# Optimization experiments

Hardware: AMD Instinct MI355X
Metric: run time of the kernel (lower is better)

## Reference

```python
import jax, jax.numpy as jnp
import numpy as np

HIDDEN = 1024
NUM_HEAD = 16
HEAD_DIM = HIDDEN // NUM_HEAD


def setup_inputs() -> dict:
    key = jax.random.key(0)
    ks = jax.random.split(key, 12)
    bs, seq = 4, 2048
    inp = {
        'srcQ': jax.random.normal(ks[0], (bs, seq, HIDDEN), jnp.float32),
        'srcK': jax.random.normal(ks[1], (bs, seq, HIDDEN), jnp.float32),
        'srcV': jax.random.normal(ks[2], (bs, seq, HIDDEN), jnp.float32),
        'mask': jnp.ones((bs, 1, 1, seq), jnp.int32),
        'Wq': jax.random.normal(ks[3], (HIDDEN, HIDDEN), jnp.float32) * 0.02,
        'bq': jnp.zeros((HIDDEN,), jnp.float32),
        'Wk': jax.random.normal(ks[4], (HIDDEN, HIDDEN), jnp.float32) * 0.02,
        'bk': jnp.zeros((HIDDEN,), jnp.float32),
        'Wv': jax.random.normal(ks[5], (HIDDEN, HIDDEN), jnp.float32) * 0.02,
        'bv': jnp.zeros((HIDDEN,), jnp.float32),
        'Wo': jax.random.normal(ks[6], (HIDDEN, HIDDEN), jnp.float32) * 0.02,
        'bo': jnp.zeros((HIDDEN,), jnp.float32),
    }
    return inp


def _split_heads(x):
    # [bs, seq, hidden] -> [bs, num_head, seq, head_dim]
    bs, seq, _ = x.shape
    return x.reshape(bs, seq, NUM_HEAD, HEAD_DIM).transpose(0, 2, 1, 3)


def reference(srcQ, srcK, srcV, mask, Wq, bq, Wk, bk, Wv, bv, Wo, bo):
    Q = _split_heads(srcQ @ Wq + bq)
    K = _split_heads(srcK @ Wk + bk)
    V = _split_heads(srcV @ Wv + bv)
    # NOTE: original module applies NO 1/sqrt(d) scaling (scale tensor unused)
    scores = jnp.einsum('bhqd,bhkd->bhqk', Q, K)
    scores = jnp.where(mask == 0, jnp.float32(-10000.0), scores)
    attn = jax.nn.softmax(scores, axis=-1)  # dropout is identity in eval
    out = jnp.einsum('bhqk,bhkd->bhqd', attn, V)
    bs, _, seq, _ = out.shape
    out = out.transpose(0, 2, 1, 3).reshape(bs, seq, HIDDEN)
    return out @ Wo + bo
```

## Files before the change

kernel.cpp:

```cpp
#include <hip/hip_runtime.h>

typedef short bf16x8 __attribute__((ext_vector_type(8)));
typedef short bf16x4 __attribute__((ext_vector_type(4)));
typedef float f32x4 __attribute__((ext_vector_type(4)));
typedef unsigned short ushort8 __attribute__((ext_vector_type(8)));
typedef unsigned short ushort4v __attribute__((ext_vector_type(4)));
typedef unsigned int uint4v __attribute__((ext_vector_type(4)));
typedef float float4v __attribute__((ext_vector_type(4)));

#define LOG2E 1.4426950408889634f
#define MASKED_VAL -14426.950408889634f

__device__ __forceinline__ unsigned short f2bf(float f) {
  unsigned u = __builtin_bit_cast(unsigned, f);
  u = u + 0x7fffu + ((u >> 16) & 1u);
  return (unsigned short)(u >> 16);
}

__device__ __forceinline__ unsigned pk2(float a, float b) {
  unsigned r;
  asm("v_cvt_pk_bf16_f32 %0, %1, %2" : "=v"(r) : "v"(a), "v"(b));
  return r;
}

__device__ __forceinline__ float exp2a(float x) {
  float r;
  asm("v_exp_f32 %0, %1" : "=v"(r) : "v"(x));
  return r;
}

__device__ __forceinline__ void gload16(const void* g, void* l) {
  __builtin_amdgcn_global_load_lds(
      (const __attribute__((address_space(1))) unsigned int*)g,
      (__attribute__((address_space(3))) unsigned int*)l, 16, 0, 0);
}

__global__ __launch_bounds__(256) void transpose_w4(const float* __restrict__ W0,
                                                    const float* __restrict__ W1,
                                                    const float* __restrict__ W2,
                                                    const float* __restrict__ W3,
                                                    unsigned short* __restrict__ Wt) {
  __shared__ float tile[32][33];
  const int z = blockIdx.z;
  const float* W = (z == 0) ? W0 : (z == 1) ? W1 : (z == 2) ? W2 : W3;
  unsigned short* o = Wt + (size_t)z * (1 << 20);
  int bx = blockIdx.x * 32;
  int by = blockIdx.y * 32;
  int tx = threadIdx.x & 31;
  int ty = threadIdx.x >> 5;
#pragma unroll
  for (int j = 0; j < 32; j += 8)
    tile[ty + j][tx] = W[(size_t)(by + ty + j) * 1024 + bx + tx];
  __syncthreads();
#pragma unroll
  for (int j = 0; j < 32; j += 8)
    o[(size_t)(bx + ty + j) * 1024 + by + tx] = f2bf(tile[tx][ty + j]);
}

__global__ __launch_bounds__(256, 3) void gemm_qkv(
    const float* __restrict__ srcQ, const float* __restrict__ srcK,
    const float* __restrict__ srcV, const unsigned short* __restrict__ Wt,
    const float* __restrict__ bq, const float* __restrict__ bk,
    const float* __restrict__ bv, unsigned short* __restrict__ Qb,
    unsigned short* __restrict__ Kb, unsigned short* __restrict__ Vt) {
  __shared__ __align__(16) unsigned short As[3][128 * 32];
  __shared__ __align__(16) unsigned short Bs[3][128 * 32];
  const int K = 1024, N = 1024;
  const int chunk = blockIdx.x >> 9;
  const int inner = blockIdx.x & 511;
  const int x = inner & 7, i = inner >> 3;
  const int bm = (x << 3) + (i >> 3);
  const int bn = i & 7;
  const float* Af = (chunk == 0) ? srcQ : (chunk == 1) ? srcK : srcV;
  const unsigned short* Bt = Wt + (size_t)chunk * (1 << 20);
  const float* bias = (chunk == 0) ? bq : (chunk == 1) ? bk : bv;
  const float scale = (chunk == 0) ? LOG2E : 1.0f;
  const int t = threadIdx.x;
  const int lane = t & 63, wid = t >> 6;
  const int wr = wid >> 1, wc = wid & 1;
  const int lr = lane & 15, lg = lane >> 4;
  f32x4 acc[4][4] = {};
  const size_t baseA = (size_t)(bm * 128) * K;
  const size_t baseB = (size_t)(bn * 128) * K;
  const int c0 = t, c1 = t + 256;
  const size_t a0off = baseA + (size_t)(c0 >> 2) * K + (c0 & 3) * 8;
  const size_t a1off = baseA + (size_t)(c1 >> 2) * K + (c1 & 3) * 8;
  const size_t b0off = baseB + (size_t)(c0 >> 2) * K + (c0 & 3) * 8;
  const size_t b1off = baseB + (size_t)(c1 >> 2) * K + (c1 & 3) * 8;

  unsigned short* pA0 = &As[0][0];
  unsigned short* pA1 = &As[1][0];
  unsigned short* pA2 = &As[2][0];
  unsigned short* pB0 = &Bs[0][0];
  unsigned short* pB1 = &Bs[1][0];
  unsigned short* pB2 = &Bs[2][0];
  float4v fE[4], fO[4];

  auto loadA = [&](float4v* f, int ks) {
    f[0] = *(const float4v*)&Af[a0off + ks];
    f[1] = *(const float4v*)&Af[a0off + ks + 4];
    f[2] = *(const float4v*)&Af[a1off + ks];
    f[3] = *(const float4v*)&Af[a1off + ks + 4];
  };
  auto writeA = [&](const float4v* f, unsigned short* dst) {
    uint4v w0, w1;
    w0[0] = pk2(f[0][0], f[0][1]); w0[1] = pk2(f[0][2], f[0][3]);
    w0[2] = pk2(f[1][0], f[1][1]); w0[3] = pk2(f[1][2], f[1][3]);
    w1[0] = pk2(f[2][0], f[2][1]); w1[1] = pk2(f[2][2], f[2][3]);
    w1[2] = pk2(f[3][0], f[3][1]); w1[3] = pk2(f[3][2], f[3][3]);
    *(uint4v*)&dst[c0 * 8] = w0;
    *(uint4v*)&dst[c1 * 8] = w1;
  };
  auto compute = [&]() {
    bf16x8 a[4], b[4];
#pragma unroll
    for (int m = 0; m < 4; ++m)
      a[m] = *(const bf16x8*)&pA0[(wr * 64 + 16 * m + lr) * 32 + lg * 8];
#pragma unroll
    for (int n = 0; n < 4; ++n)
      b[n] = *(const bf16x8*)&pB0[(wc * 64 + 16 * n + lr) * 32 + lg * 8];
    __builtin_amdgcn_s_setprio(1);
#pragma unroll
    for (int m = 0; m < 4; ++m)
#pragma unroll
      for (int n = 0; n < 4; ++n)
        acc[m][n] = __builtin_amdgcn_mfma_f32_16x16x32_bf16(a[m], b[n], acc[m][n], 0, 0, 0);
    __builtin_amdgcn_s_setprio(0);
  };
  auto rotate = [&]() {
    unsigned short* ta = pA0; pA0 = pA1; pA1 = pA2; pA2 = ta;
    unsigned short* tb = pB0; pB0 = pB1; pB1 = pB2; pB2 = tb;
  };

  gload16(&Bt[b0off], &pB0[c0 * 8]);
  gload16(&Bt[b1off], &pB0[c1 * 8]);
  loadA(fE, 0);
  gload16(&Bt[b0off + 32], &pB1[c0 * 8]);
  gload16(&Bt[b1off + 32], &pB1[c1 * 8]);
  loadA(fO, 32);
  writeA(fE, pA0);
  asm volatile("s_waitcnt lgkmcnt(0)" ::: "memory");
  __builtin_amdgcn_s_barrier();

  for (int it = 0; it < 16; ++it) {
    const int ks0 = 64 * it;
    if (it < 15) {
      gload16(&Bt[b0off + ks0 + 64], &pB2[c0 * 8]);
      gload16(&Bt[b1off + ks0 + 64], &pB2[c1 * 8]);
      loadA(fE, ks0 + 64);
    }
    compute();
    writeA(fO, pA1);
    asm volatile("s_waitcnt lgkmcnt(0)" ::: "memory");
    __builtin_amdgcn_sched_barrier(0);
    __builtin_amdgcn_s_barrier();
    rotate();
    if (it < 15) {
      gload16(&Bt[b0off + ks0 + 96], &pB2[c0 * 8]);
      gload16(&Bt[b1off + ks0 + 96], &pB2[c1 * 8]);
      loadA(fO, ks0 + 96);
    }
    compute();
    if (it < 15) {
      writeA(fE, pA1);
      asm volatile("s_waitcnt lgkmcnt(0)" ::: "memory");
      __builtin_amdgcn_sched_barrier(0);
      __builtin_amdgcn_s_barrier();
      rotate();
    }
  }

  const int rowb = bm * 128 + wr * 64;
  const int colb = bn * 128 + wc * 64;
  if (chunk == 2) {
    const int bidx = rowb >> 11;
    const int srow = rowb & 2047;
#pragma unroll
    for (int n = 0; n < 4; ++n) {
      int col = colb + 16 * n + lr;
      float bv_ = bias[col];
#pragma unroll
      for (int m = 0; m < 4; ++m) {
        int s0 = srow + 16 * m + 4 * lg;
        ushort4v u;
#pragma unroll
        for (int r = 0; r < 4; ++r) u[r] = f2bf(acc[m][n][r] + bv_);
        *(ushort4v*)&Vt[((size_t)(bidx * 1024 + col)) * 2048 + s0] = u;
      }
    }
  } else {
    unsigned short* C = (chunk == 0) ? Qb : Kb;
#pragma unroll
    for (int n = 0; n < 4; ++n) {
      int col = colb + 16 * n + lr;
      float bv_ = bias[col];
#pragma unroll
      for (int m = 0; m < 4; ++m) {
        int row0 = rowb + 16 * m + 4 * lg;
#pragma unroll
        for (int r = 0; r < 4; ++r)
          C[(size_t)(row0 + r) * N + col] = f2bf((acc[m][n][r] + bv_) * scale);
      }
    }
  }
}

__global__ __launch_bounds__(256, 3) void gemm_out(const unsigned short* __restrict__ A,
                                                   const unsigned short* __restrict__ Bt,
                                                   const float* __restrict__ bias,
                                                   float* __restrict__ C) {
  __shared__ __align__(16) unsigned short As[3][128 * 32];
  __shared__ __align__(16) unsigned short Bs[3][128 * 32];
  const int K = 1024, N = 1024;
  const int x = blockIdx.x & 7, i = blockIdx.x >> 3;
  const int bm = (x << 3) + (i >> 3);
  const int bn = i & 7;
  const int t = threadIdx.x;
  const int lane = t & 63, wid = t >> 6;
  const int wr = wid >> 1, wc = wid & 1;
  const int lr = lane & 15, lg = lane >> 4;
  f32x4 acc[4][4] = {};
  const size_t baseA = (size_t)(bm * 128) * K;
  const size_t baseB = (size_t)(bn * 128) * K;
  const int c0 = t, c1 = t + 256;
  const size_t a0off = baseA + (size_t)(c0 >> 2) * K + (c0 & 3) * 8;
  const size_t a1off = baseA + (size_t)(c1 >> 2) * K + (c1 & 3) * 8;
  const size_t b0off = baseB + (size_t)(c0 >> 2) * K + (c0 & 3) * 8;
  const size_t b1off = baseB + (size_t)(c1 >> 2) * K + (c1 & 3) * 8;

  unsigned short* pA0 = &As[0][0];
  unsigned short* pA1 = &As[1][0];
  unsigned short* pA2 = &As[2][0];
  unsigned short* pB0 = &Bs[0][0];
  unsigned short* pB1 = &Bs[1][0];
  unsigned short* pB2 = &Bs[2][0];

  auto issue = [&](int ks, unsigned short* dA, unsigned short* dB) {
    gload16(&A[a0off + ks], &dA[c0 * 8]);
    gload16(&A[a1off + ks], &dA[c1 * 8]);
    gload16(&Bt[b0off + ks], &dB[c0 * 8]);
    gload16(&Bt[b1off + ks], &dB[c1 * 8]);
  };
  auto rotate = [&]() {
    unsigned short* ta = pA0; pA0 = pA1; pA1 = pA2; pA2 = ta;
    unsigned short* tb = pB0; pB0 = pB1; pB1 = pB2; pB2 = tb;
  };

  issue(0, pA0, pB0);
  issue(32, pA1, pB1);
  asm volatile("s_waitcnt vmcnt(4)" ::: "memory");
  __builtin_amdgcn_sched_barrier(0);
  __builtin_amdgcn_s_barrier();

  for (int tt = 0; tt < 32; ++tt) {
    if (tt < 30) issue(32 * tt + 64, pA2, pB2);
    bf16x8 a[4], b[4];
#pragma unroll
    for (int m = 0; m < 4; ++m)
      a[m] = *(const bf16x8*)&pA0[(wr * 64 + 16 * m + lr) * 32 + lg * 8];
#pragma unroll
    for (int n = 0; n < 4; ++n)
      b[n] = *(const bf16x8*)&pB0[(wc * 64 + 16 * n + lr) * 32 + lg * 8];
    __builtin_amdgcn_s_setprio(1);
#pragma unroll
    for (int m = 0; m < 4; ++m)
#pragma unroll
      for (int n = 0; n < 4; ++n)
        acc[m][n] = __builtin_amdgcn_mfma_f32_16x16x32_bf16(a[m], b[n], acc[m][n], 0, 0, 0);
    __builtin_amdgcn_s_setprio(0);
    if (tt < 31) {
      if (tt < 30) {
        asm volatile("s_waitcnt vmcnt(4)" ::: "memory");
      } else {
        asm volatile("s_waitcnt vmcnt(0)" ::: "memory");
      }
      __builtin_amdgcn_sched_barrier(0);
      __builtin_amdgcn_s_barrier();
      rotate();
    }
  }

  const int rowb = bm * 128 + wr * 64;
  const int colb = bn * 128 + wc * 64;
#pragma unroll
  for (int n = 0; n < 4; ++n) {
    int col = colb + 16 * n + lr;
    float bv = bias[col];
#pragma unroll
    for (int m = 0; m < 4; ++m) {
      int row0 = rowb + 16 * m + 4 * lg;
#pragma unroll
      for (int r = 0; r < 4; ++r)
        C[(size_t)(row0 + r) * N + col] = acc[m][n][r] + bv;
    }
  }
}

__global__ __launch_bounds__(256, 4) void attn_kernel(
    const unsigned short* __restrict__ Q, const unsigned short* __restrict__ K,
    const unsigned short* __restrict__ V, const int* __restrict__ mask,
    unsigned short* __restrict__ ctx) {
  __shared__ __align__(16) unsigned short pool[16384];
  __shared__ int s_any[4];
  unsigned short* Kbuf0 = pool;
  unsigned short* Kbuf1 = pool + 4096;
  unsigned short* Vbuf0 = pool + 8192;
  unsigned short* Vbuf1 = pool + 12288;
  const int g = blockIdx.x;
  const int bid = (g & 7) * 128 + (g >> 3);
  const int qb = bid & 15, h = (bid >> 4) & 15, b = bid >> 8;
  const int t = threadIdx.x;
  const int lane = t & 63, wid = t >> 6;
  const int lr = lane & 15, lg = lane >> 4;
  const size_t rowQ0 = (size_t)(b * 2048 + qb * 128);
  const int hcol = h * 64;
  const size_t vrow0 = (size_t)((b * 16 + h) * 64) * 2048;

  size_t ksrc[2], vsrc[2];
  int ldso[2];
#pragma unroll
  for (int i = 0; i < 2; ++i) {
    int ci = t + 256 * i;
    int row = ci >> 3, pos = ci & 7;
    ksrc[i] = (size_t)(b * 2048 + row) * 1024 + hcol + ((pos ^ (row & 7)) << 3);
    vsrc[i] = vrow0 + (size_t)row * 2048 + ((pos ^ ((row >> 1) & 7)) << 3);
    ldso[i] = ci * 8;
  }
#pragma unroll
  for (int i = 0; i < 4; ++i) {
    int ci = t + 256 * i;
    int row = ci >> 3, pos = ci & 7;
    gload16(&Q[(rowQ0 + row) * 1024 + hcol + ((pos ^ (row & 7)) << 3)], &pool[ci * 8]);
  }
  int bad = 0;
  const int* mb = mask + b * 2048;
#pragma unroll
  for (int i = 0; i < 2; ++i) {
    int4 mv = *(const int4*)&mb[t * 8 + i * 4];
    bad |= (mv.x == 0) | (mv.y == 0) | (mv.z == 0) | (mv.w == 0);
  }
  unsigned long long bb = __ballot(bad);
  if (lane == 0) s_any[wid] = (bb != 0ULL);
  __syncthreads();
  bf16x8 aq[2][2];
#pragma unroll
  for (int m = 0; m < 2; ++m)
#pragma unroll
    for (int kd = 0; kd < 2; ++kd) {
      int row = wid * 32 + 16 * m + lr;
      int ch = (4 * kd + lg) ^ (lr & 7);
      aq[m][kd] = *(const bf16x8*)&pool[row * 64 + ch * 8];
    }
  const bool anymask = (s_any[0] | s_any[1] | s_any[2] | s_any[3]) != 0;
  __syncthreads();
#pragma unroll
  for (int i = 0; i < 2; ++i) gload16(&K[ksrc[i]], &Kbuf0[ldso[i]]);
#pragma unroll
  for (int i = 0; i < 2; ++i) gload16(&V[vsrc[i]], &Vbuf0[ldso[i]]);
  __syncthreads();

  f32x4 o[2][4] = {};
  f32x4 ol[2] = {};
  const short oneb = 0x3F80;
  const bf16x8 ones8 = {oneb, oneb, oneb, oneb, oneb, oneb, oneb, oneb};
  const f32x4 zero4 = {0.f, 0.f, 0.f, 0.f};
  const int ch0 = (lg ^ (lr & 7)) * 8;
  const int ch1 = ((4 + lg) ^ (lr & 7)) * 8;
  const int sw = lr >> 1;

  for (int kb = 0; kb < 32; ++kb) {
    const int bi = kb & 1;
    const unsigned short* Kb_ = bi ? Kbuf1 : Kbuf0;
    const unsigned short* Vb_ = bi ? Vbuf1 : Vbuf0;
    unsigned short* Kn_ = bi ? Kbuf0 : Kbuf1;
    unsigned short* Vn_ = bi ? Vbuf0 : Vbuf1;
    if (kb + 1 < 32) {
      const size_t ko = (size_t)(kb + 1) * 64 * 1024;
      const size_t vo = (size_t)(kb + 1) * 64;
#pragma unroll
      for (int i = 0; i < 2; ++i) gload16(&K[ksrc[i] + ko], &Kn_[ldso[i]]);
#pragma unroll
      for (int i = 0; i < 2; ++i) gload16(&V[vsrc[i] + vo], &Vn_[ldso[i]]);
    }
    f32x4 s[2][4];
    __builtin_amdgcn_s_setprio(1);
#pragma unroll
    for (int n = 0; n < 4; ++n) {
      bf16x8 k0 = *(const bf16x8*)&Kb_[(16 * n + lr) * 64 + ch0];
      bf16x8 k1 = *(const bf16x8*)&Kb_[(16 * n + lr) * 64 + ch1];
      f32x4 t0 = __builtin_amdgcn_mfma_f32_16x16x32_bf16(k0, aq[0][0], zero4, 0, 0, 0);
      s[0][n] = __builtin_amdgcn_mfma_f32_16x16x32_bf16(k1, aq[0][1], t0, 0, 0, 0);
      f32x4 t1 = __builtin_amdgcn_mfma_f32_16x16x32_bf16(k0, aq[1][0], zero4, 0, 0, 0);
      s[1][n] = __builtin_amdgcn_mfma_f32_16x16x32_bf16(k1, aq[1][1], t1, 0, 0, 0);
    }
    __builtin_amdgcn_s_setprio(0);
    if (anymask) {
      const int* mrow = mb + kb * 64;
#pragma unroll
      for (int n = 0; n < 4; ++n) {
        int4 mv = *(const int4*)&mrow[16 * n + 4 * lg];
        int mm[4] = {mv.x, mv.y, mv.z, mv.w};
#pragma unroll
        for (int r = 0; r < 4; ++r)
          if (mm[r] == 0) { s[0][n][r] = MASKED_VAL; s[1][n][r] = MASKED_VAL; }
      }
    }
#pragma unroll
    for (int m = 0; m < 2; ++m)
#pragma unroll
      for (int n = 0; n < 4; ++n)
#pragma unroll
        for (int r = 0; r < 4; ++r) s[m][n][r] = exp2a(s[m][n][r]);
#pragma unroll
    for (int kk = 0; kk < 2; ++kk) {
      bf16x8 pf[2];
#pragma unroll
      for (int m = 0; m < 2; ++m) {
        uint4v u;
        u[0] = pk2(s[m][2 * kk][0], s[m][2 * kk][1]);
        u[1] = pk2(s[m][2 * kk][2], s[m][2 * kk][3]);
        u[2] = pk2(s[m][2 * kk + 1][0], s[m][2 * kk + 1][1]);
        u[3] = pk2(s[m][2 * kk + 1][2], s[m][2 * kk + 1][3]);
        pf[m] = __builtin_bit_cast(bf16x8, u);
      }
      __builtin_amdgcn_s_setprio(1);
      ol[0] = __builtin_amdgcn_mfma_f32_16x16x32_bf16(ones8, pf[0], ol[0], 0, 0, 0);
      ol[1] = __builtin_amdgcn_mfma_f32_16x16x32_bf16(ones8, pf[1], ol[1], 0, 0, 0);
      const int p0 = (4 * kk + (lg >> 1)) ^ sw;
      const int base0 = lr * 64 + p0 * 8 + (lg & 1) * 4;
      const int base1 = lr * 64 + (p0 ^ 2) * 8 + (lg & 1) * 4;
#pragma unroll
      for (int dn = 0; dn < 4; ++dn) {
        bf16x4 v0 = *(const bf16x4*)&Vb_[base0 + dn * 1024];
        bf16x4 v1 = *(const bf16x4*)&Vb_[base1 + dn * 1024];
        bf16x8 vb = __builtin_shufflevector(v0, v1, 0, 1, 2, 3, 4, 5, 6, 7);
#pragma unroll
        for (int m = 0; m < 2; ++m)
          o[m][dn] = __builtin_amdgcn_mfma_f32_16x16x32_bf16(vb, pf[m], o[m][dn], 0, 0, 0);
      }
      __builtin_amdgcn_s_setprio(0);
    }
    __syncthreads();
  }
#pragma unroll
  for (int m = 0; m < 2; ++m) {
    float inv = 1.f / ol[m][0];
    size_t q = rowQ0 + wid * 32 + 16 * m + lr;
#pragma unroll
    for (int dn = 0; dn < 4; ++dn) {
      ushort4v u;
#pragma unroll
      for (int r = 0; r < 4; ++r) u[r] = f2bf(o[m][dn][r] * inv);
      *(ushort4v*)&ctx[q * 1024 + hcol + 16 * dn + 4 * lg] = u;
    }
  }
}

extern "C" void kernel_launch(void* const* d_in, const int* in_sizes, int n_in,
                              void* d_out, int out_size, void* d_ws, size_t ws_size,
                              hipStream_t stream) {
  const float* srcQ = (const float*)d_in[0];
  const float* srcK = (const float*)d_in[1];
  const float* srcV = (const float*)d_in[2];
  const int*   mask = (const int*)d_in[3];
  const float* Wq = (const float*)d_in[4];
  const float* bq = (const float*)d_in[5];
  const float* Wk = (const float*)d_in[6];
  const float* bk = (const float*)d_in[7];
  const float* Wv = (const float*)d_in[8];
  const float* bv = (const float*)d_in[9];
  const float* Wo = (const float*)d_in[10];
  const float* bo = (const float*)d_in[11];
  float* out = (float*)d_out;

  char* ws = (char*)d_ws;
  unsigned short* ctx = (unsigned short*)(ws);
  unsigned short* Qb  = (unsigned short*)(ws + (size_t)(16 << 20));
  unsigned short* Kb  = (unsigned short*)(ws + (size_t)(32 << 20));
  unsigned short* Vt  = (unsigned short*)(ws + (size_t)(48 << 20));
  unsigned short* Wt  = (unsigned short*)(ws + (size_t)(64 << 20));

  transpose_w4<<<dim3(32, 32, 4), 256, 0, stream>>>(Wq, Wk, Wv, Wo, Wt);

  gemm_qkv<<<1536, 256, 0, stream>>>(srcQ, srcK, srcV, Wt, bq, bk, bv, Qb, Kb, Vt);

  attn_kernel<<<1024, 256, 0, stream>>>(Qb, Kb, Vt, mask, ctx);

  gemm_out<<<512, 256, 0, stream>>>(ctx, Wt + 3 * (1 << 20), bo, out);
}
```

Before: 180.9 us.

## Double attention block to 256 query rows with 8 waves sharing K/V tiles

The attention kernel now runs 512 threads (8 waves) per block and covers 256 query rows instead of 128. Each K/V tile staged in shared memory is reused by twice as many waves, which halves global K/V traffic and the number of load instructions per thread. The cost is half as many blocks (512), so fewer independent blocks fill the CUs and each block synchronises more waves. The launch bound of 512x4 may also constrain registers.

```diff
diff --git a/kernel.cpp b/kernel.cpp
--- a/kernel.cpp
+++ b/kernel.cpp
@@ -296,49 +296,40 @@
   }
 }
 
-__global__ __launch_bounds__(256, 4) void attn_kernel(
+__global__ __launch_bounds__(512, 4) void attn_kernel(
     const unsigned short* __restrict__ Q, const unsigned short* __restrict__ K,
     const unsigned short* __restrict__ V, const int* __restrict__ mask,
     unsigned short* __restrict__ ctx) {
   __shared__ __align__(16) unsigned short pool[16384];
-  __shared__ int s_any[4];
+  __shared__ int s_any[8];
   unsigned short* Kbuf0 = pool;
   unsigned short* Kbuf1 = pool + 4096;
   unsigned short* Vbuf0 = pool + 8192;
   unsigned short* Vbuf1 = pool + 12288;
   const int g = blockIdx.x;
-  const int bid = (g & 7) * 128 + (g >> 3);
-  const int qb = bid & 15, h = (bid >> 4) & 15, b = bid >> 8;
+  const int bid = (g & 7) * 64 + (g >> 3);
+  const int qb = bid & 7, h = (bid >> 3) & 15, b = bid >> 7;
   const int t = threadIdx.x;
   const int lane = t & 63, wid = t >> 6;
   const int lr = lane & 15, lg = lane >> 4;
-  const size_t rowQ0 = (size_t)(b * 2048 + qb * 128);
+  const size_t rowQ0 = (size_t)(b * 2048 + qb * 256);
   const int hcol = h * 64;
   const size_t vrow0 = (size_t)((b * 16 + h) * 64) * 2048;
 
-  size_t ksrc[2], vsrc[2];
-  int ldso[2];
-#pragma unroll
-  for (int i = 0; i < 2; ++i) {
-    int ci = t + 256 * i;
-    int row = ci >> 3, pos = ci & 7;
-    ksrc[i] = (size_t)(b * 2048 + row) * 1024 + hcol + ((pos ^ (row & 7)) << 3);
-    vsrc[i] = vrow0 + (size_t)row * 2048 + ((pos ^ ((row >> 1) & 7)) << 3);
-    ldso[i] = ci * 8;
-  }
+  const int row_s = t >> 3, pos_s = t & 7;
+  const size_t ksrc = (size_t)(b * 2048 + row_s) * 1024 + hcol + ((pos_s ^ (row_s & 7)) << 3);
+  const size_t vsrc = vrow0 + (size_t)row_s * 2048 + ((pos_s ^ ((row_s >> 1) & 7)) << 3);
+  const int ldso = t * 8;
+
 #pragma unroll
   for (int i = 0; i < 4; ++i) {
-    int ci = t + 256 * i;
+    int ci = t + 512 * i;
     int row = ci >> 3, pos = ci & 7;
     gload16(&Q[(rowQ0 + row) * 1024 + hcol + ((pos ^ (row & 7)) << 3)], &pool[ci * 8]);
   }
-  int bad = 0;
   const int* mb = mask + b * 2048;
-#pragma unroll
-  for (int i = 0; i < 2; ++i) {
-    int4 mv = *(const int4*)&mb[t * 8 + i * 4];
-    bad |= (mv.x == 0) | (mv.y == 0) | (mv.z == 0) | (mv.w == 0);
-  }
+  int4 mv0 = *(const int4*)&mb[t * 4];
+  int bad = (mv0.x == 0) | (mv0.y == 0) | (mv0.z == 0) | (mv0.w == 0);
   unsigned long long bb = __ballot(bad);
   if (lane == 0) s_any[wid] = (bb != 0ULL);
   __syncthreads();
@@ -351,12 +342,13 @@
       int ch = (4 * kd + lg) ^ (lr & 7);
       aq[m][kd] = *(const bf16x8*)&pool[row * 64 + ch * 8];
     }
-  const bool anymask = (s_any[0] | s_any[1] | s_any[2] | s_any[3]) != 0;
+  int anyi = 0;
+#pragma unroll
+  for (int w = 0; w < 8; ++w) anyi |= s_any[w];
+  const bool anymask = anyi != 0;
   __syncthreads();
-#pragma unroll
-  for (int i = 0; i < 2; ++i) gload16(&K[ksrc[i]], &Kbuf0[ldso[i]]);
-#pragma unroll
-  for (int i = 0; i < 2; ++i) gload16(&V[vsrc[i]], &Vbuf0[ldso[i]]);
+  gload16(&K[ksrc], &Kbuf0[ldso]);
+  gload16(&V[vsrc], &Vbuf0[ldso]);
   __syncthreads();
 
   f32x4 o[2][4] = {};
@@ -375,12 +367,8 @@
     unsigned short* Kn_ = bi ? Kbuf0 : Kbuf1;
     unsigned short* Vn_ = bi ? Vbuf0 : Vbuf1;
     if (kb + 1 < 32) {
-      const size_t ko = (size_t)(kb + 1) * 64 * 1024;
-      const size_t vo = (size_t)(kb + 1) * 64;
-#pragma unroll
-      for (int i = 0; i < 2; ++i) gload16(&K[ksrc[i] + ko], &Kn_[ldso[i]]);
-#pragma unroll
-      for (int i = 0; i < 2; ++i) gload16(&V[vsrc[i] + vo], &Vn_[ldso[i]]);
+      gload16(&K[ksrc + (size_t)(kb + 1) * 64 * 1024], &Kn_[ldso]);
+      gload16(&V[vsrc + (size_t)(kb + 1) * 64], &Vn_[ldso]);
     }
     f32x4 s[2][4];
     __builtin_amdgcn_s_setprio(1);
@@ -484,7 +472,7 @@
 
   gemm_qkv<<<1536, 256, 0, stream>>>(srcQ, srcK, srcV, Wt, bq, bk, bv, Qb, Kb, Vt);
 
-  attn_kernel<<<1024, 256, 0, stream>>>(Qb, Kb, Vt, mask, ctx);
+  attn_kernel<<<512, 512, 0, stream>>>(Qb, Kb, Vt, mask, ctx);
 
   gemm_out<<<512, 256, 0, stream>>>(ctx, Wt + 3 * (1 << 20), bo, out);
 }
```

Result: no change. 177.9 us (-1.7%).
